# Performance work log

Hardware: AMD Instinct MI355X
Metric: run time of the kernel (lower is better)

## Reference

```python
import jax, jax.numpy as jnp
import numpy as np

B, N, M, D_IN, D_OUT, H = 4, 2048, 2048, 512, 512, 8
HD = D_OUT // H
LN_EPS = 1e-5


def setup_inputs() -> dict:
    key = jax.random.key(0)
    ks = jax.random.split(key, 10)
    query = jax.random.normal(ks[0], (B, N, D_IN), dtype=jnp.float32)
    kee = jax.random.normal(ks[1], (B, M, D_IN), dtype=jnp.float32)
    val = jax.random.normal(ks[2], (B, M, D_IN), dtype=jnp.float32)
    mask = jax.random.randint(ks[3], (B, N, M), 0, 2, dtype=jnp.int32)
    # xavier_uniform with gain 1/sqrt(2): limit = gain * sqrt(6/(fan_in+fan_out))
    lim = (1.0 / np.sqrt(2.0)) * np.sqrt(6.0 / (D_IN + D_OUT))
    WQ = jax.random.uniform(ks[4], (D_OUT, D_IN), jnp.float32, -lim, lim)
    WK = jax.random.uniform(ks[5], (D_OUT, D_IN), jnp.float32, -lim, lim)
    WV = jax.random.uniform(ks[6], (D_OUT, D_IN), jnp.float32, -lim, lim)
    limO = (1.0 / np.sqrt(2.0)) * np.sqrt(6.0 / (D_OUT + D_OUT))
    WO = jax.random.uniform(ks[7], (D_OUT, D_OUT), jnp.float32, -limO, limO)
    bO = jnp.zeros((D_OUT,), jnp.float32)
    gamma = jnp.ones((D_OUT,), jnp.float32)
    beta = jnp.zeros((D_OUT,), jnp.float32)
    return {"query": query, "key": kee, "value": val, "mask": mask,
            "WQ": WQ, "WK": WK, "WV": WV, "WO": WO, "bO": bO,
            "gamma": gamma, "beta": beta}


def reference(query, key, value, mask, WQ, WK, WV, WO, bO, gamma, beta):
    scale = jnp.float32(1.0 / np.sqrt(HD))
    # project and split heads: [B, H, S, HD]
    Q = (query @ WQ.T).reshape(B, N, H, HD).transpose(0, 2, 1, 3)
    K = (key @ WK.T).reshape(B, M, H, HD).transpose(0, 2, 1, 3)
    V = (value @ WV.T).reshape(B, M, H, HD).transpose(0, 2, 1, 3)
    attn = jnp.einsum('bhnd,bhmd->bhnm', Q, K) * scale
    attn = jnp.where(mask[:, None, :, :] == 0, -jnp.inf, attn)
    attn = jax.nn.softmax(attn, axis=-1)  # dropout is identity in eval
    out = jnp.einsum('bhnm,bhmd->bhnd', attn, V)
    out = out.transpose(0, 2, 1, 3).reshape(B, N, D_OUT)
    out = out @ WO.T + bO
    x = out + query  # residual_proj is Identity (input_dim == output_dim)
    mu = jnp.mean(x, axis=-1, keepdims=True)
    var = jnp.var(x, axis=-1, keepdims=True)
    return (x - mu) * jax.lax.rsqrt(var + LN_EPS) * gamma + beta
```

## Files before the change

kernel.cpp:

```cpp
#include <hip/hip_runtime.h>
#include <stdint.h>

#define B_   4
#define N_   2048
#define M_   2048
#define DIN  512
#define DOUT 512
#define H_   8
#define HD_  64
#define ROWS (B_ * N_)

typedef __attribute__((ext_vector_type(8))) short bf16x8;
typedef __attribute__((ext_vector_type(4))) float f32x4;
typedef __attribute__((ext_vector_type(2))) unsigned int u32x2;
typedef unsigned short u16;
typedef unsigned int   u32;

#if __has_builtin(__builtin_amdgcn_exp2f)
#define EXP2(x) __builtin_amdgcn_exp2f(x)
#else
#define EXP2(x) exp2f(x)
#endif

__device__ __forceinline__ u16 f2bf(float x) {
  union { float f; u32 u; } v; v.f = x;
  u32 r = (v.u + 0x7FFFu + ((v.u >> 16) & 1u)) >> 16;
  return (u16)r;
}

__device__ __forceinline__ u32 pkbf(float a, float b) {
  u32 r;
  asm("v_cvt_pk_bf16_f32 %0, %1, %2" : "=v"(r) : "v"(a), "v"(b));
  return r;
}

__device__ __forceinline__ void gld16(u16* lds, const u16* g) {
  __builtin_amdgcn_global_load_lds((const __attribute__((address_space(1))) u32*)g,
                                   (__attribute__((address_space(3))) u32*)lds, 16, 0, 0);
}

__global__ __launch_bounds__(256) void k_prep(
    const float* __restrict__ q, const float* __restrict__ k, const float* __restrict__ v,
    const float* __restrict__ wq_, const float* __restrict__ wk_,
    const float* __restrict__ wv_, const float* __restrict__ wo_,
    const int* __restrict__ mask,
    u16* __restrict__ qb, u16* __restrict__ kb, u16* __restrict__ vb,
    u16* __restrict__ wqb, u16* __restrict__ wkb, u16* __restrict__ wvb, u16* __restrict__ wob,
    u32* __restrict__ mbits)
{
  const int id = blockIdx.x;
  if (id >= 6656) {
    const int id2 = id - 6656;
    const int lane = threadIdx.x & 63;
    const int gw = id2 * 4 + (threadIdx.x >> 6);
    #pragma unroll 4
    for (int it = 0; it < 32; ++it) {
      long pos = ((long)(it * 8192 + gw)) * 64 + lane;
      int mv = mask[pos];
      unsigned long long bal = __ballot(mv != 0);
      if ((lane & 31) == 0) mbits[pos >> 5] = (u32)(bal >> lane);
    }
    return;
  }
  const float* s; u16* d; size_t i;
  if (id < 6144) {
    const int seg = id >> 11;
    s = seg == 0 ? q : seg == 1 ? k : v;
    d = seg == 0 ? qb : seg == 1 ? kb : vb;
    i = (size_t)(id & 2047) * 2048 + threadIdx.x * 8;
  } else {
    const int wid = id - 6144;
    const int seg = wid >> 7;
    s = seg == 0 ? wq_ : seg == 1 ? wk_ : seg == 2 ? wv_ : wo_;
    d = seg == 0 ? wqb : seg == 1 ? wkb : seg == 2 ? wvb : wob;
    i = (size_t)(wid & 127) * 2048 + threadIdx.x * 8;
  }
  f32x4 x = *(const f32x4*)(s + i);
  f32x4 y = *(const f32x4*)(s + i + 4);
  bf16x8 r;
  r[0] = (short)f2bf(x[0]); r[1] = (short)f2bf(x[1]);
  r[2] = (short)f2bf(x[2]); r[3] = (short)f2bf(x[3]);
  r[4] = (short)f2bf(y[0]); r[5] = (short)f2bf(y[1]);
  r[6] = (short)f2bf(y[2]); r[7] = (short)f2bf(y[3]);
  *(bf16x8*)(d + i) = r;
}

__global__ __launch_bounds__(256) void k_gemm_qkv(
    const u16* __restrict__ Aq, const u16* __restrict__ Ak, const u16* __restrict__ Av,
    const u16* __restrict__ Wq, const u16* __restrict__ Wk, const u16* __restrict__ Wv,
    u16* __restrict__ Qo, u16* __restrict__ Ko, u16* __restrict__ Vt)
{
  __shared__ __align__(16) u16 At[128 * 64];
  __shared__ __align__(16) u16 Bt[128 * 64];
  const int z = blockIdx.z;
  const u16* A = z == 0 ? Aq : z == 1 ? Ak : Av;
  const u16* W = z == 0 ? Wq : z == 1 ? Wk : Wv;
  const int bm = blockIdx.y, bn = blockIdx.x;
  const int t = threadIdx.x, l = t & 63;
  const int w = t >> 6, wr = w >> 1, wc = w & 1;
  const int l15 = l & 15, lg = l >> 4;
  f32x4 acc[4][4] = {};
  const u16* ga = A + (size_t)(bm * 128 + (t >> 3)) * DIN + (t & 7) * 8;
  const u16* gb = W + (size_t)(bn * 128 + (t >> 3)) * DIN + (t & 7) * 8;
  u16* la = &At[t * 8];
  u16* lb = &Bt[t * 8];
  const u16* rowT = (z < 2) ? &Bt[wc * 64 * 64] : &At[wr * 64 * 64];
  const u16* colT = (z < 2) ? &At[wr * 64 * 64] : &Bt[wc * 64 * 64];
  for (int kt = 0; kt < 8; ++kt) {
    const int k0 = kt * 64;
    #pragma unroll
    for (int s2 = 0; s2 < 4; ++s2) {
      gld16(la + s2 * 2048, ga + (size_t)s2 * 32 * DIN + k0);
      gld16(lb + s2 * 2048, gb + (size_t)s2 * 32 * DIN + k0);
    }
    __syncthreads();
    bf16x8 rf[4][2], cf[4][2];
    #pragma unroll
    for (int i = 0; i < 4; ++i)
      #pragma unroll
      for (int c = 0; c < 2; ++c)
        rf[i][c] = *(const bf16x8*)&rowT[(i * 16 + l15) * 64 + c * 32 + lg * 8];
    #pragma unroll
    for (int j = 0; j < 4; ++j)
      #pragma unroll
      for (int c = 0; c < 2; ++c)
        cf[j][c] = *(const bf16x8*)&colT[(j * 16 + l15) * 64 + c * 32 + lg * 8];
    #pragma unroll
    for (int i = 0; i < 4; ++i)
      #pragma unroll
      for (int j = 0; j < 4; ++j) {
        acc[i][j] = __builtin_amdgcn_mfma_f32_16x16x32_bf16(rf[i][0], cf[j][0], acc[i][j], 0, 0, 0);
        acc[i][j] = __builtin_amdgcn_mfma_f32_16x16x32_bf16(rf[i][1], cf[j][1], acc[i][j], 0, 0, 0);
      }
    __syncthreads();
  }
  if (z < 2) {
    u16* C = z == 0 ? Qo : Ko;
    const float scl = z == 0 ? 0.18033688f : 1.0f;
    #pragma unroll
    for (int i = 0; i < 4; ++i) {
      const int o0 = bn * 128 + wc * 64 + i * 16 + lg * 4;
      #pragma unroll
      for (int j = 0; j < 4; ++j) {
        const int m = bm * 128 + wr * 64 + j * 16 + l15;
        u32x2 pr;
        pr[0] = pkbf(acc[i][j][0] * scl, acc[i][j][1] * scl);
        pr[1] = pkbf(acc[i][j][2] * scl, acc[i][j][3] * scl);
        *(u32x2*)&C[(size_t)m * DOUT + o0] = pr;
      }
    }
  } else {
    #pragma unroll
    for (int i = 0; i < 4; ++i) {
      const int mm = bm * 128 + wr * 64 + i * 16 + lg * 4;
      const int bb = mm >> 11, s = mm & 2047;
      #pragma unroll
      for (int j = 0; j < 4; ++j) {
        const int o = bn * 128 + wc * 64 + j * 16 + l15;
        u32x2 pr;
        pr[0] = pkbf(acc[i][j][0], acc[i][j][1]);
        pr[1] = pkbf(acc[i][j][2], acc[i][j][3]);
        *(u32x2*)&Vt[(size_t)(bb * 512 + o) * M_ + s] = pr;
      }
    }
  }
}

__global__ __launch_bounds__(256) void k_attn(
    const u16* __restrict__ Qp, const u16* __restrict__ Kp, const u16* __restrict__ Vt,
    const u32* __restrict__ mbits, u16* __restrict__ AO)
{
  __shared__ __align__(16) u16 KT[2][64 * 64];
  __shared__ __align__(16) u16 VT[2][64 * 64];
  const int qt = blockIdx.x, bh = blockIdx.y;
  const int b = bh >> 3, h = bh & 7;
  const int t = threadIdx.x, l = t & 63, w = t >> 6;
  const int l15 = l & 15, lg = l >> 4;

  const int srow = t >> 3;
  const int scol8 = t & 7;
  const int scol = (scol8 ^ (srow & 7)) * 8;
  const int kpr = (srow >> 5) * 32 + (((srow >> 4) & 1) * 4) + (((srow & 15) >> 2) * 8) + (srow & 3);
  const u16* gK = Kp + (size_t)(b * N_ + kpr) * DOUT + h * HD_ + scol;
  const u16* gV = Vt + (size_t)(b * 512 + h * HD_ + srow) * M_ + scol;

  const int qrow = qt * 64 + w * 16 + l15;
  const bf16x8 qf0 = *(const bf16x8*)&Qp[((size_t)(b * N_) + qrow) * DOUT + h * HD_ + lg * 8];
  const bf16x8 qf1 = *(const bf16x8*)&Qp[((size_t)(b * N_) + qrow) * DOUT + h * HD_ + 32 + lg * 8];
  const u32* mrow = mbits + ((size_t)(b * N_) + qrow) * (M_ / 32);

  f32x4 o[4] = {};
  f32x4 lacc = {};
  union U8 { u32 u[4]; bf16x8 v; };
  U8 ones;
  ones.u[0] = ones.u[1] = ones.u[2] = ones.u[3] = 0x3F803F80u;

  #define STAGE(buf_, m0_) do {                                   \
    const u16* gk_ = gK + (size_t)(m0_) * DOUT;                   \
    const u16* gv_ = gV + (m0_);                                  \
    u16* lk_ = &KT[buf_][t * 8];                                  \
    u16* lv_ = &VT[buf_][t * 8];                                  \
    gld16(lk_, gk_);                                              \
    gld16(lk_ + 2048, gk_ + (size_t)32 * DOUT);                   \
    gld16(lv_, gv_);                                              \
    gld16(lv_ + 2048, gv_ + (size_t)32 * M_);                     \
  } while (0)

  STAGE(0, 0);
  __syncthreads();

  for (int it = 0; it < 32; ++it) {
    const int buf = it & 1;
    const int m0 = it * 64;
    if (it + 1 < 32) STAGE(buf ^ 1, m0 + 64);

    const u32 mw0 = mrow[m0 >> 5];
    const u32 mw1 = mrow[(m0 >> 5) + 1];

    const u16* Kb = KT[buf];
    const u16* Vb = VT[buf];
    const int xs = l15 & 7;

    U8 pa[2];
    #pragma unroll
    for (int kbk = 0; kbk < 2; ++kbk) {
      f32x4 sS[2];
      #pragma unroll
      for (int u = 0; u < 2; ++u) {
        const int row = kbk * 32 + u * 16 + l15;
        const bf16x8 a0 = *(const bf16x8*)&Kb[row * 64 + ((lg ^ xs) * 8)];
        const bf16x8 a1 = *(const bf16x8*)&Kb[row * 64 + (((4 + lg) ^ xs) * 8)];
        f32x4 zz = {};
        zz = __builtin_amdgcn_mfma_f32_16x16x32_bf16(a0, qf0, zz, 0, 0, 0);
        zz = __builtin_amdgcn_mfma_f32_16x16x32_bf16(a1, qf1, zz, 0, 0, 0);
        sS[u] = zz;
      }
      const u32 mw = kbk ? mw1 : mw0;
      float e[8];
      #pragma unroll
      for (int u = 0; u < 2; ++u)
        #pragma unroll
        for (int r = 0; r < 4; ++r) {
          const int bit = lg * 8 + u * 4 + r;
          float p = EXP2(sS[u][r]);
          e[u * 4 + r] = ((mw >> bit) & 1u) ? p : 0.f;
        }
      pa[kbk].u[0] = pkbf(e[0], e[1]);
      pa[kbk].u[1] = pkbf(e[2], e[3]);
      pa[kbk].u[2] = pkbf(e[4], e[5]);
      pa[kbk].u[3] = pkbf(e[6], e[7]);
    }
    lacc = __builtin_amdgcn_mfma_f32_16x16x32_bf16(ones.v, pa[0].v, lacc, 0, 0, 0);
    lacc = __builtin_amdgcn_mfma_f32_16x16x32_bf16(ones.v, pa[1].v, lacc, 0, 0, 0);

    #pragma unroll
    for (int nd = 0; nd < 4; ++nd) {
      const int vrow = nd * 16 + l15;
      const bf16x8 vb0 = *(const bf16x8*)&Vb[vrow * 64 + ((lg ^ xs) * 8)];
      const bf16x8 vb1 = *(const bf16x8*)&Vb[vrow * 64 + (((4 + lg) ^ xs) * 8)];
      o[nd] = __builtin_amdgcn_mfma_f32_16x16x32_bf16(vb0, pa[0].v, o[nd], 0, 0, 0);
      o[nd] = __builtin_amdgcn_mfma_f32_16x16x32_bf16(vb1, pa[1].v, o[nd], 0, 0, 0);
    }
    __syncthreads();
  }

  const float ls = lacc[0];
  const float rq = ls > 0.f ? 1.f / ls : 0.f;
  const size_t obase = ((size_t)(b * N_) + qrow) * DOUT + h * HD_;
  #pragma unroll
  for (int nd = 0; nd < 4; ++nd) {
    u32x2 pr;
    pr[0] = pkbf(o[nd][0] * rq, o[nd][1] * rq);
    pr[1] = pkbf(o[nd][2] * rq, o[nd][3] * rq);
    *(u32x2*)&AO[obase + nd * 16 + lg * 4] = pr;
  }
  #undef STAGE
}

__global__ __launch_bounds__(256) void k_gemm_out(
    const u16* __restrict__ A, const u16* __restrict__ W,
    const float* __restrict__ bO, const float* __restrict__ query,
    float* __restrict__ X)
{
  __shared__ __align__(16) u16 At[128 * 64];
  __shared__ __align__(16) u16 Bt[128 * 64];
  const int bm = blockIdx.y, bn = blockIdx.x;
  const int t = threadIdx.x, l = t & 63;
  const int w = t >> 6, wr = w >> 1, wc = w & 1;
  const int l15 = l & 15, lg = l >> 4;
  f32x4 acc[4][4] = {};
  const u16* ga = A + (size_t)(bm * 128 + (t >> 3)) * DOUT + (t & 7) * 8;
  const u16* gb = W + (size_t)(bn * 128 + (t >> 3)) * DOUT + (t & 7) * 8;
  u16* la = &At[t * 8];
  u16* lb = &Bt[t * 8];
  const u16* rowT = &Bt[wc * 64 * 64];
  const u16* colT = &At[wr * 64 * 64];
  for (int kt = 0; kt < 8; ++kt) {
    const int k0 = kt * 64;
    #pragma unroll
    for (int s2 = 0; s2 < 4; ++s2) {
      gld16(la + s2 * 2048, ga + (size_t)s2 * 32 * DOUT + k0);
      gld16(lb + s2 * 2048, gb + (size_t)s2 * 32 * DOUT + k0);
    }
    __syncthreads();
    bf16x8 rf[4][2], cf[4][2];
    #pragma unroll
    for (int i = 0; i < 4; ++i)
      #pragma unroll
      for (int c = 0; c < 2; ++c)
        rf[i][c] = *(const bf16x8*)&rowT[(i * 16 + l15) * 64 + c * 32 + lg * 8];
    #pragma unroll
    for (int j = 0; j < 4; ++j)
      #pragma unroll
      for (int c = 0; c < 2; ++c)
        cf[j][c] = *(const bf16x8*)&colT[(j * 16 + l15) * 64 + c * 32 + lg * 8];
    #pragma unroll
    for (int i = 0; i < 4; ++i)
      #pragma unroll
      for (int j = 0; j < 4; ++j) {
        acc[i][j] = __builtin_amdgcn_mfma_f32_16x16x32_bf16(rf[i][0], cf[j][0], acc[i][j], 0, 0, 0);
        acc[i][j] = __builtin_amdgcn_mfma_f32_16x16x32_bf16(rf[i][1], cf[j][1], acc[i][j], 0, 0, 0);
      }
    __syncthreads();
  }
  #pragma unroll
  for (int i = 0; i < 4; ++i) {
    const int o0 = bn * 128 + wc * 64 + i * 16 + lg * 4;
    const f32x4 bo4 = *(const f32x4*)&bO[o0];
    #pragma unroll
    for (int j = 0; j < 4; ++j) {
      const int m = bm * 128 + wr * 64 + j * 16 + l15;
      const size_t idx = (size_t)m * DOUT + o0;
      const f32x4 qv = *(const f32x4*)&query[idx];
      f32x4 res;
      #pragma unroll
      for (int r = 0; r < 4; ++r) res[r] = acc[i][j][r] + bo4[r] + qv[r];
      *(f32x4*)&X[idx] = res;
    }
  }
}

__global__ __launch_bounds__(256) void k_ln(
    const float* __restrict__ X, const float* __restrict__ gamma,
    const float* __restrict__ beta, float* __restrict__ out)
{
  const int w = threadIdx.x >> 6, l = threadIdx.x & 63;
  const int row = blockIdx.x * 4 + w;
  const float* x = X + (size_t)row * DOUT + l * 8;
  f32x4 a = *(const f32x4*)(x);
  f32x4 b = *(const f32x4*)(x + 4);
  float s = a[0] + a[1] + a[2] + a[3] + b[0] + b[1] + b[2] + b[3];
  float q = a[0]*a[0] + a[1]*a[1] + a[2]*a[2] + a[3]*a[3]
          + b[0]*b[0] + b[1]*b[1] + b[2]*b[2] + b[3]*b[3];
  #pragma unroll
  for (int m = 1; m < 64; m <<= 1) { s += __shfl_xor(s, m); q += __shfl_xor(q, m); }
  const float mean = s * (1.f / 512.f);
  const float var = q * (1.f / 512.f) - mean * mean;
  const float rstd = rsqrtf(var + 1e-5f);
  f32x4 g1 = *(const f32x4*)(gamma + l * 8);
  f32x4 g2 = *(const f32x4*)(gamma + l * 8 + 4);
  f32x4 e1 = *(const f32x4*)(beta + l * 8);
  f32x4 e2 = *(const f32x4*)(beta + l * 8 + 4);
  f32x4 r1, r2;
  #pragma unroll
  for (int i = 0; i < 4; ++i) {
    r1[i] = (a[i] - mean) * rstd * g1[i] + e1[i];
    r2[i] = (b[i] - mean) * rstd * g2[i] + e2[i];
  }
  float* op = out + (size_t)row * DOUT + l * 8;
  *(f32x4*)(op) = r1;
  *(f32x4*)(op + 4) = r2;
}

extern "C" void kernel_launch(void* const* d_in, const int* in_sizes, int n_in,
                              void* d_out, int out_size, void* d_ws, size_t ws_size,
                              hipStream_t stream)
{
  const float* query = (const float*)d_in[0];
  const float* key   = (const float*)d_in[1];
  const float* value = (const float*)d_in[2];
  const int*   mask  = (const int*)d_in[3];
  const float* WQ    = (const float*)d_in[4];
  const float* WK    = (const float*)d_in[5];
  const float* WV    = (const float*)d_in[6];
  const float* WO    = (const float*)d_in[7];
  const float* bO    = (const float*)d_in[8];
  const float* gamma = (const float*)d_in[9];
  const float* beta  = (const float*)d_in[10];
  float* out = (float*)d_out;

  char* ws = (char*)d_ws;
  size_t off = 0;
  auto alloc = [&](size_t bytes) -> char* {
    char* p = ws + off;
    off += (bytes + 255) & ~(size_t)255;
    return p;
  };
  u16* qb  = (u16*)alloc((size_t)ROWS * DIN * 2);
  u16* kb  = (u16*)alloc((size_t)ROWS * DIN * 2);
  u16* vb  = (u16*)alloc((size_t)ROWS * DIN * 2);
  u16* wq  = (u16*)alloc((size_t)DOUT * DIN * 2);
  u16* wk  = (u16*)alloc((size_t)DOUT * DIN * 2);
  u16* wv  = (u16*)alloc((size_t)DOUT * DIN * 2);
  u16* wo  = (u16*)alloc((size_t)DOUT * DIN * 2);
  u16* Qp  = (u16*)alloc((size_t)ROWS * DOUT * 2);
  u16* Kp  = (u16*)alloc((size_t)ROWS * DOUT * 2);
  u16* Vt  = (u16*)alloc((size_t)ROWS * DOUT * 2);
  u32* mb  = (u32*)alloc((size_t)B_ * N_ * (M_ / 32) * 4);
  u16* AO  = (u16*)alloc((size_t)ROWS * DOUT * 2);
  float* X = (float*)alloc((size_t)ROWS * DOUT * 4);

  k_prep     <<<8704, 256, 0, stream>>>(query, key, value, WQ, WK, WV, WO, mask,
                                        qb, kb, vb, wq, wk, wv, wo, mb);
  k_gemm_qkv <<<dim3(4, 64, 3), 256, 0, stream>>>(qb, kb, vb, wq, wk, wv, Qp, Kp, Vt);
  k_attn     <<<dim3(32, 32), 256, 0, stream>>>(Qp, Kp, Vt, mb, AO);
  k_gemm_out <<<dim3(4, 64), 256, 0, stream>>>(AO, wo, bO, query, X);
  k_ln       <<<2048, 256, 0, stream>>>(X, gamma, beta, out);
}
```

Measured before the change: 274.7 us.

## Double-buffer GEMMs, triple-buffer attention, spread mask packing, use bf16 residual and LN input

Both GEMM kernels now double-buffer their LDS tiles, so the next K-slice loads while the current one is multiplied. The attention kernel moves to a three-stage K/V ring with explicit vmcnt waits and raw barriers, and it prefetches the next mask words. The mask-packing part of the prep kernel now uses many more blocks, each doing fewer iterations. The residual path reads the bf16 copy of query instead of fp32 and writes X as bf16 into reused workspace, so LayerNorm reads half the bytes. This lowers residual and LN-input precision, and the hand-written waitcnt counts must exactly match the number of outstanding loads.

```diff
diff --git a/kernel.cpp b/kernel.cpp
--- a/kernel.cpp
+++ b/kernel.cpp
@@ -13,6 +13,7 @@
 typedef __attribute__((ext_vector_type(8))) short bf16x8;
 typedef __attribute__((ext_vector_type(4))) float f32x4;
 typedef __attribute__((ext_vector_type(2))) unsigned int u32x2;
+typedef __attribute__((ext_vector_type(4))) unsigned short u16x4;
 typedef unsigned short u16;
 typedef unsigned int   u32;
 
@@ -26,6 +27,11 @@
   union { float f; u32 u; } v; v.f = x;
   u32 r = (v.u + 0x7FFFu + ((v.u >> 16) & 1u)) >> 16;
   return (u16)r;
+}
+
+__device__ __forceinline__ float bf2f(u16 x) {
+  union { u32 u; float f; } v; v.u = ((u32)x) << 16;
+  return v.f;
 }
 
 __device__ __forceinline__ u32 pkbf(float a, float b) {
@@ -53,9 +59,9 @@
     const int id2 = id - 6656;
     const int lane = threadIdx.x & 63;
     const int gw = id2 * 4 + (threadIdx.x >> 6);
-    #pragma unroll 4
-    for (int it = 0; it < 32; ++it) {
-      long pos = ((long)(it * 8192 + gw)) * 64 + lane;
+    #pragma unroll
+    for (int it2 = 0; it2 < 4; ++it2) {
+      long pos = ((long)gw * 4 + it2) * 64 + lane;
       int mv = mask[pos];
       unsigned long long bal = __ballot(mv != 0);
       if ((lane & 31) == 0) mbits[pos >> 5] = (u32)(bal >> lane);
@@ -90,8 +96,8 @@
     const u16* __restrict__ Wq, const u16* __restrict__ Wk, const u16* __restrict__ Wv,
     u16* __restrict__ Qo, u16* __restrict__ Ko, u16* __restrict__ Vt)
 {
-  __shared__ __align__(16) u16 At[128 * 64];
-  __shared__ __align__(16) u16 Bt[128 * 64];
+  __shared__ __align__(16) u16 At[2][128 * 64];
+  __shared__ __align__(16) u16 Bt[2][128 * 64];
   const int z = blockIdx.z;
   const u16* A = z == 0 ? Aq : z == 1 ? Ak : Av;
   const u16* W = z == 0 ? Wq : z == 1 ? Wk : Wv;
@@ -102,18 +108,24 @@
   f32x4 acc[4][4] = {};
   const u16* ga = A + (size_t)(bm * 128 + (t >> 3)) * DIN + (t & 7) * 8;
   const u16* gb = W + (size_t)(bn * 128 + (t >> 3)) * DIN + (t & 7) * 8;
-  u16* la = &At[t * 8];
-  u16* lb = &Bt[t * 8];
-  const u16* rowT = (z < 2) ? &Bt[wc * 64 * 64] : &At[wr * 64 * 64];
-  const u16* colT = (z < 2) ? &At[wr * 64 * 64] : &Bt[wc * 64 * 64];
+
+  #define STG(buf_, k0_) do {                                           \
+    u16* la_ = &At[buf_][t * 8];                                        \
+    u16* lb_ = &Bt[buf_][t * 8];                                        \
+    _Pragma("unroll")                                                   \
+    for (int s2 = 0; s2 < 4; ++s2) {                                    \
+      gld16(la_ + s2 * 2048, ga + (size_t)s2 * 32 * DIN + (k0_));       \
+      gld16(lb_ + s2 * 2048, gb + (size_t)s2 * 32 * DIN + (k0_));       \
+    }                                                                   \
+  } while (0)
+
+  STG(0, 0);
+  __syncthreads();
   for (int kt = 0; kt < 8; ++kt) {
-    const int k0 = kt * 64;
-    #pragma unroll
-    for (int s2 = 0; s2 < 4; ++s2) {
-      gld16(la + s2 * 2048, ga + (size_t)s2 * 32 * DIN + k0);
-      gld16(lb + s2 * 2048, gb + (size_t)s2 * 32 * DIN + k0);
-    }
-    __syncthreads();
+    const int buf = kt & 1;
+    if (kt + 1 < 8) STG(buf ^ 1, (kt + 1) * 64);
+    const u16* rowT = (z < 2) ? &Bt[buf][wc * 64 * 64] : &At[buf][wr * 64 * 64];
+    const u16* colT = (z < 2) ? &At[buf][wr * 64 * 64] : &Bt[buf][wc * 64 * 64];
     bf16x8 rf[4][2], cf[4][2];
     #pragma unroll
     for (int i = 0; i < 4; ++i)
@@ -134,6 +146,7 @@
       }
     __syncthreads();
   }
+  #undef STG
   if (z < 2) {
     u16* C = z == 0 ? Qo : Ko;
     const float scl = z == 0 ? 0.18033688f : 1.0f;
@@ -170,8 +183,8 @@
     const u16* __restrict__ Qp, const u16* __restrict__ Kp, const u16* __restrict__ Vt,
     const u32* __restrict__ mbits, u16* __restrict__ AO)
 {
-  __shared__ __align__(16) u16 KT[2][64 * 64];
-  __shared__ __align__(16) u16 VT[2][64 * 64];
+  __shared__ __align__(16) u16 KT[3][64 * 64];
+  __shared__ __align__(16) u16 VT[3][64 * 64];
   const int qt = blockIdx.x, bh = blockIdx.y;
   const int b = bh >> 3, h = bh & 7;
   const int t = threadIdx.x, l = t & 63, w = t >> 6;
@@ -206,21 +219,26 @@
     gld16(lv_ + 2048, gv_ + (size_t)32 * M_);                     \
   } while (0)
 
+  u32x2 mc = *(const u32x2*)&mrow[0];
   STAGE(0, 0);
-  __syncthreads();
+  STAGE(1, 64);
+  __builtin_amdgcn_sched_barrier(0);
+  asm volatile("s_waitcnt vmcnt(4)" ::: "memory");
+  __builtin_amdgcn_sched_barrier(0);
+  __builtin_amdgcn_s_barrier();
+  __builtin_amdgcn_sched_barrier(0);
 
   for (int it = 0; it < 32; ++it) {
-    const int buf = it & 1;
-    const int m0 = it * 64;
-    if (it + 1 < 32) STAGE(buf ^ 1, m0 + 64);
-
-    const u32 mw0 = mrow[m0 >> 5];
-    const u32 mw1 = mrow[(m0 >> 5) + 1];
-
-    const u16* Kb = KT[buf];
-    const u16* Vb = VT[buf];
+    const int cur = it % 3;
+    const u16* Kb = KT[cur];
+    const u16* Vb = VT[cur];
+
+    u32x2 mn = {0u, 0u};
+    if (it + 1 < 32) mn = *(const u32x2*)&mrow[2 * (it + 1)];
+    if (it + 2 < 32) STAGE((it + 2) % 3, (it + 2) * 64);
+    __builtin_amdgcn_sched_barrier(0);
+
     const int xs = l15 & 7;
-
     U8 pa[2];
     #pragma unroll
     for (int kbk = 0; kbk < 2; ++kbk) {
@@ -235,7 +253,7 @@
         zz = __builtin_amdgcn_mfma_f32_16x16x32_bf16(a1, qf1, zz, 0, 0, 0);
         sS[u] = zz;
       }
-      const u32 mw = kbk ? mw1 : mw0;
+      const u32 mw = kbk ? mc[1] : mc[0];
       float e[8];
       #pragma unroll
       for (int u = 0; u < 2; ++u)
@@ -252,7 +270,6 @@
     }
     lacc = __builtin_amdgcn_mfma_f32_16x16x32_bf16(ones.v, pa[0].v, lacc, 0, 0, 0);
     lacc = __builtin_amdgcn_mfma_f32_16x16x32_bf16(ones.v, pa[1].v, lacc, 0, 0, 0);
-
     #pragma unroll
     for (int nd = 0; nd < 4; ++nd) {
       const int vrow = nd * 16 + l15;
@@ -261,7 +278,20 @@
       o[nd] = __builtin_amdgcn_mfma_f32_16x16x32_bf16(vb0, pa[0].v, o[nd], 0, 0, 0);
       o[nd] = __builtin_amdgcn_mfma_f32_16x16x32_bf16(vb1, pa[1].v, o[nd], 0, 0, 0);
     }
-    __syncthreads();
+    mc = mn;
+
+    __builtin_amdgcn_sched_barrier(0);
+    if (it < 30) {
+      asm volatile("s_waitcnt vmcnt(5)" ::: "memory");
+      __builtin_amdgcn_sched_barrier(0);
+      __builtin_amdgcn_s_barrier();
+      __builtin_amdgcn_sched_barrier(0);
+    } else if (it == 30) {
+      asm volatile("s_waitcnt vmcnt(1)" ::: "memory");
+      __builtin_amdgcn_sched_barrier(0);
+      __builtin_amdgcn_s_barrier();
+      __builtin_amdgcn_sched_barrier(0);
+    }
   }
 
   const float ls = lacc[0];
@@ -279,11 +309,11 @@
 
 __global__ __launch_bounds__(256) void k_gemm_out(
     const u16* __restrict__ A, const u16* __restrict__ W,
-    const float* __restrict__ bO, const float* __restrict__ query,
-    float* __restrict__ X)
-{
-  __shared__ __align__(16) u16 At[128 * 64];
-  __shared__ __align__(16) u16 Bt[128 * 64];
+    const float* __restrict__ bO, const u16* __restrict__ qb,
+    u16* __restrict__ X)
+{
+  __shared__ __align__(16) u16 At[2][128 * 64];
+  __shared__ __align__(16) u16 Bt[2][128 * 64];
   const int bm = blockIdx.y, bn = blockIdx.x;
   const int t = threadIdx.x, l = t & 63;
   const int w = t >> 6, wr = w >> 1, wc = w & 1;
@@ -291,18 +321,24 @@
   f32x4 acc[4][4] = {};
   const u16* ga = A + (size_t)(bm * 128 + (t >> 3)) * DOUT + (t & 7) * 8;
   const u16* gb = W + (size_t)(bn * 128 + (t >> 3)) * DOUT + (t & 7) * 8;
-  u16* la = &At[t * 8];
-  u16* lb = &Bt[t * 8];
-  const u16* rowT = &Bt[wc * 64 * 64];
-  const u16* colT = &At[wr * 64 * 64];
+
+  #define STG(buf_, k0_) do {                                           \
+    u16* la_ = &At[buf_][t * 8];                                        \
+    u16* lb_ = &Bt[buf_][t * 8];                                        \
+    _Pragma("unroll")                                                   \
+    for (int s2 = 0; s2 < 4; ++s2) {                                    \
+      gld16(la_ + s2 * 2048, ga + (size_t)s2 * 32 * DOUT + (k0_));      \
+      gld16(lb_ + s2 * 2048, gb + (size_t)s2 * 32 * DOUT + (k0_));      \
+    }                                                                   \
+  } while (0)
+
+  STG(0, 0);
+  __syncthreads();
   for (int kt = 0; kt < 8; ++kt) {
-    const int k0 = kt * 64;
-    #pragma unroll
-    for (int s2 = 0; s2 < 4; ++s2) {
-      gld16(la + s2 * 2048, ga + (size_t)s2 * 32 * DOUT + k0);
-      gld16(lb + s2 * 2048, gb + (size_t)s2 * 32 * DOUT + k0);
-    }
-    __syncthreads();
+    const int buf = kt & 1;
+    if (kt + 1 < 8) STG(buf ^ 1, (kt + 1) * 64);
+    const u16* rowT = &Bt[buf][wc * 64 * 64];
+    const u16* colT = &At[buf][wr * 64 * 64];
     bf16x8 rf[4][2], cf[4][2];
     #pragma unroll
     for (int i = 0; i < 4; ++i)
@@ -323,6 +359,7 @@
       }
     __syncthreads();
   }
+  #undef STG
   #pragma unroll
   for (int i = 0; i < 4; ++i) {
     const int o0 = bn * 128 + wc * 64 + i * 16 + lg * 4;
@@ -331,27 +368,28 @@
     for (int j = 0; j < 4; ++j) {
       const int m = bm * 128 + wr * 64 + j * 16 + l15;
       const size_t idx = (size_t)m * DOUT + o0;
-      const f32x4 qv = *(const f32x4*)&query[idx];
-      f32x4 res;
-      #pragma unroll
-      for (int r = 0; r < 4; ++r) res[r] = acc[i][j][r] + bo4[r] + qv[r];
-      *(f32x4*)&X[idx] = res;
+      const u16x4 qv = *(const u16x4*)&qb[idx];
+      u32x2 pr;
+      pr[0] = pkbf(acc[i][j][0] + bo4[0] + bf2f(qv[0]), acc[i][j][1] + bo4[1] + bf2f(qv[1]));
+      pr[1] = pkbf(acc[i][j][2] + bo4[2] + bf2f(qv[2]), acc[i][j][3] + bo4[3] + bf2f(qv[3]));
+      *(u32x2*)&X[idx] = pr;
     }
   }
 }
 
 __global__ __launch_bounds__(256) void k_ln(
-    const float* __restrict__ X, const float* __restrict__ gamma,
+    const u16* __restrict__ X, const float* __restrict__ gamma,
     const float* __restrict__ beta, float* __restrict__ out)
 {
   const int w = threadIdx.x >> 6, l = threadIdx.x & 63;
   const int row = blockIdx.x * 4 + w;
-  const float* x = X + (size_t)row * DOUT + l * 8;
-  f32x4 a = *(const f32x4*)(x);
-  f32x4 b = *(const f32x4*)(x + 4);
-  float s = a[0] + a[1] + a[2] + a[3] + b[0] + b[1] + b[2] + b[3];
-  float q = a[0]*a[0] + a[1]*a[1] + a[2]*a[2] + a[3]*a[3]
-          + b[0]*b[0] + b[1]*b[1] + b[2]*b[2] + b[3]*b[3];
+  const bf16x8 xv = *(const bf16x8*)(X + (size_t)row * DOUT + l * 8);
+  float xf[8];
+  #pragma unroll
+  for (int i = 0; i < 8; ++i) xf[i] = bf2f((u16)xv[i]);
+  float s = 0.f, q = 0.f;
+  #pragma unroll
+  for (int i = 0; i < 8; ++i) { s += xf[i]; q += xf[i] * xf[i]; }
   #pragma unroll
   for (int m = 1; m < 64; m <<= 1) { s += __shfl_xor(s, m); q += __shfl_xor(q, m); }
   const float mean = s * (1.f / 512.f);
@@ -364,8 +402,8 @@
   f32x4 r1, r2;
   #pragma unroll
   for (int i = 0; i < 4; ++i) {
-    r1[i] = (a[i] - mean) * rstd * g1[i] + e1[i];
-    r2[i] = (b[i] - mean) * rstd * g2[i] + e2[i];
+    r1[i] = (xf[i] - mean) * rstd * g1[i] + e1[i];
+    r2[i] = (xf[i + 4] - mean) * rstd * g2[i] + e2[i];
   }
   float* op = out + (size_t)row * DOUT + l * 8;
   *(f32x4*)(op) = r1;
@@ -407,13 +445,13 @@
   u16* Kp  = (u16*)alloc((size_t)ROWS * DOUT * 2);
   u16* Vt  = (u16*)alloc((size_t)ROWS * DOUT * 2);
   u32* mb  = (u32*)alloc((size_t)B_ * N_ * (M_ / 32) * 4);
-  u16* AO  = (u16*)alloc((size_t)ROWS * DOUT * 2);
-  float* X = (float*)alloc((size_t)ROWS * DOUT * 4);
-
-  k_prep     <<<8704, 256, 0, stream>>>(query, key, value, WQ, WK, WV, WO, mask,
-                                        qb, kb, vb, wq, wk, wv, wo, mb);
+  u16* AO  = vb;
+  u16* X   = kb;
+
+  k_prep     <<<23040, 256, 0, stream>>>(query, key, value, WQ, WK, WV, WO, mask,
+                                         qb, kb, vb, wq, wk, wv, wo, mb);
   k_gemm_qkv <<<dim3(4, 64, 3), 256, 0, stream>>>(qb, kb, vb, wq, wk, wv, Qp, Kp, Vt);
   k_attn     <<<dim3(32, 32), 256, 0, stream>>>(Qp, Kp, Vt, mb, AO);
-  k_gemm_out <<<dim3(4, 64), 256, 0, stream>>>(AO, wo, bO, query, X);
+  k_gemm_out <<<dim3(4, 64), 256, 0, stream>>>(AO, wo, bO, qb, X);
   k_ln       <<<2048, 256, 0, stream>>>(X, gamma, beta, out);
 }
```

Result: slower. 287.1 us (+4.5%).
